# Optimization experiments

Measured on AMD Instinct MI355X. Metric: run time of the kernel, lower is better.

The kernel has to match this reference:

```python
import math
import jax, jax.numpy as jnp
import numpy as np

D_MODEL = 1024
N_HEADS = 16
HEAD_DIM = D_MODEL // N_HEADS
D_FF = 4096
N_LAYERS = 4
VOCAB = 2048
NUM_GROUPS = 15
CACHE_LEN = 17  # positions 0..16
EPS = 1e-6


def rmsnorm(x, w):
    return x * w * jax.lax.rsqrt(jnp.mean(x * x, axis=-1, keepdims=True) + EPS)


def rope(x, pos):
    # x: [S, H, hd], pos: [S] int
    hd = x.shape[-1]
    inv = 1.0 / (10000.0 ** (jnp.arange(0, hd, 2, dtype=jnp.float32) / hd))
    ang = pos[:, None].astype(jnp.float32) * inv  # [S, hd/2]
    cos = jnp.cos(ang)[:, None, :]
    sin = jnp.sin(ang)[:, None, :]
    x1, x2 = x[..., ::2], x[..., 1::2]
    return jnp.stack([x1 * cos - x2 * sin, x1 * sin + x2 * cos], axis=-1).reshape(x.shape)


def transformer_step(x, positions, kc, vc, wq, wk, wv, wo, w1, w2, w3, ln1, ln2, lnf):
    # x: [S, d]; positions: [S] contiguous; kc/vc: [L, H, T, hd] KV caches
    S = x.shape[0]
    cache_pos = jnp.arange(CACHE_LEN)
    mask = cache_pos[None, None, :] <= positions[None, :, None]  # causal vs cache [1,S,T]
    start = positions[0]
    for l in range(N_LAYERS):
        h = rmsnorm(x, ln1[l])
        q = rope((h @ wq[l].T).reshape(S, N_HEADS, HEAD_DIM), positions)
        k = rope((h @ wk[l].T).reshape(S, N_HEADS, HEAD_DIM), positions)
        v = (h @ wv[l].T).reshape(S, N_HEADS, HEAD_DIM)
        kc = jax.lax.dynamic_update_slice(kc, k.transpose(1, 0, 2)[None], (l, 0, start, 0))
        vc = jax.lax.dynamic_update_slice(vc, v.transpose(1, 0, 2)[None], (l, 0, start, 0))
        scores = jnp.einsum('shd,htd->hst', q, kc[l]) / math.sqrt(HEAD_DIM)
        p = jax.nn.softmax(jnp.where(mask, scores, -1e30), axis=-1)
        attn = jnp.einsum('hst,htd->shd', p, vc[l]).reshape(S, D_MODEL)
        x = x + attn @ wo[l].T
        h = rmsnorm(x, ln2[l])
        x = x + (jax.nn.silu(h @ w1[l].T) * (h @ w3[l].T)) @ w2[l].T
    return rmsnorm(x, lnf), kc, vc


def forward(talker_hidden, code_0_embed, wq, wk, wv, wo, w1, w2, w3, ln1, ln2, lnf, heads, embeds):
    kc = jnp.zeros((N_LAYERS, N_HEADS, CACHE_LEN, HEAD_DIM), jnp.float32)
    vc = kc
    # prefill: [talker_hidden; code_0_embed] at positions 0,1
    x0 = jnp.concatenate([talker_hidden[0], code_0_embed[0]], axis=0)  # [2, d]
    h, kc, vc = transformer_step(x0, jnp.arange(2), kc, vc, wq, wk, wv, wo, w1, w2, w3, ln1, ln2, lnf)
    hidden = h[-1:]  # last-token hidden [1, d]

    def step(carry, xs):
        hidden, kc, vc = carry
        head, etab, pos = xs  # head/etab: [V, d]
        logits = hidden @ head.T          # [1, V]
        code = jnp.argmax(logits, axis=-1)  # [1]
        emb = etab[code]                   # [1, d]
        nh, kc, vc = transformer_step(emb, pos[None], kc, vc, wq, wk, wv, wo, w1, w2, w3, ln1, ln2, lnf)
        return (nh, kc, vc), (logits[0], emb[0])

    (_, _, _), (all_logits, embs) = jax.lax.scan(
        step, (hidden, kc, vc), (heads, embeds, jnp.arange(2, 2 + NUM_GROUPS)))
    embed_sum = code_0_embed.reshape(-1) + embs.sum(0)
    return all_logits, embed_sum  # [15, V], [d]


def setup_inputs() -> dict:
    key = jax.random.key(0)
    ks = jax.random.split(key, 16)
    s = 0.02
    f32 = jnp.float32
    return {
        'talker_hidden': jax.random.normal(ks[0], (1, 1, D_MODEL), f32),
        'code_0_embed': jax.random.normal(ks[1], (1, 1, D_MODEL), f32),
        'wq': jax.random.normal(ks[2], (N_LAYERS, D_MODEL, D_MODEL), f32) * s,
        'wk': jax.random.normal(ks[3], (N_LAYERS, D_MODEL, D_MODEL), f32) * s,
        'wv': jax.random.normal(ks[4], (N_LAYERS, D_MODEL, D_MODEL), f32) * s,
        'wo': jax.random.normal(ks[5], (N_LAYERS, D_MODEL, D_MODEL), f32) * s,
        'w1': jax.random.normal(ks[6], (N_LAYERS, D_FF, D_MODEL), f32) * s,
        'w2': jax.random.normal(ks[7], (N_LAYERS, D_MODEL, D_FF), f32) * s,
        'w3': jax.random.normal(ks[8], (N_LAYERS, D_FF, D_MODEL), f32) * s,
        'ln1': jnp.ones((N_LAYERS, D_MODEL), f32),
        'ln2': jnp.ones((N_LAYERS, D_MODEL), f32),
        'lnf': jnp.ones((D_MODEL,), f32),
        'heads': jax.random.normal(ks[9], (NUM_GROUPS, VOCAB, D_MODEL), f32) * s,
        'embeds': jax.random.normal(ks[10], (NUM_GROUPS, VOCAB, D_MODEL), f32) * s,
    }


def reference(talker_hidden, code_0_embed, wq, wk, wv, wo, w1, w2, w3, ln1, ln2, lnf, heads, embeds):
    return forward(talker_hidden, code_0_embed, wq, wk, wv, wo, w1, w2, w3, ln1, ln2, lnf, heads, embeds)
```

## Files before the change

### kernel.cpp

```cpp
#include <hip/hip_runtime.h>
#include <math.h>

#define D_MODEL 1024
#define N_HEADS 16
#define HEAD_DIM 64
#define D_FF 4096
#define N_LAYERS 4
#define VOCAB 2048
#define NUM_GROUPS 15
#define CACHE_LEN 17
#define EPS 1e-6f
#define NB 256
#define NT 1024

typedef unsigned short ushort8v __attribute__((ext_vector_type(8)));

__device__ __forceinline__ float ldc(const float* p) {
  return __hip_atomic_load((float*)p, __ATOMIC_RELAXED, __HIP_MEMORY_SCOPE_AGENT);
}
__device__ __forceinline__ void stc(float* p, float v) {
  __hip_atomic_store(p, v, __ATOMIC_RELAXED, __HIP_MEMORY_SCOPE_AGENT);
}
__device__ __forceinline__ void stc2(float* p, float a, float b) {
  union { unsigned long long u; float2 f; } c;
  c.f = make_float2(a, b);
  __hip_atomic_store((unsigned long long*)p, c.u, __ATOMIC_RELAXED,
                     __HIP_MEMORY_SCOPE_AGENT);
}
__device__ __forceinline__ void stc_u64(unsigned long long* p, unsigned long long v) {
  __hip_atomic_store(p, v, __ATOMIC_RELAXED, __HIP_MEMORY_SCOPE_AGENT);
}
__device__ __forceinline__ unsigned ldu(const unsigned* p) {
  return __hip_atomic_load((unsigned*)p, __ATOMIC_RELAXED, __HIP_MEMORY_SCOPE_AGENT);
}

__device__ __forceinline__ float bf2f(unsigned short u) {
  union { unsigned int i; float f; } c;
  c.i = ((unsigned int)u) << 16;
  return c.f;
}
__device__ __forceinline__ unsigned short f2bf(float f) {
  union { float f; unsigned int i; } c;
  c.f = f;
  unsigned int r = (c.i + 0x7fffu + ((c.i >> 16) & 1u)) >> 16;
  return (unsigned short)r;
}

__device__ __forceinline__ float wred(float v) {
#pragma unroll
  for (int o = 32; o > 0; o >>= 1) v += __shfl_xor(v, o, 64);
  return v;
}
__device__ __forceinline__ float wredmax(float v) {
#pragma unroll
  for (int o = 32; o > 0; o >>= 1) v = fmaxf(v, __shfl_xor(v, o, 64));
  return v;
}

__device__ __forceinline__ void gsync_begin(unsigned* flags, unsigned gen) {
  __syncthreads();
  if (threadIdx.x == 0)
    __hip_atomic_store(flags + (size_t)blockIdx.x * 16u, gen, __ATOMIC_RELAXED,
                       __HIP_MEMORY_SCOPE_AGENT);
}
__device__ __forceinline__ void gsync_end(unsigned* flags, unsigned gen) {
  if (threadIdx.x < 64) {
    const unsigned* f = flags + (size_t)threadIdx.x * 16u;
    for (;;) {
      unsigned a0 = ldu(f);
      unsigned a1 = ldu(f + 64 * 16);
      unsigned a2 = ldu(f + 128 * 16);
      unsigned a3 = ldu(f + 192 * 16);
      if (a0 >= gen && a1 >= gen && a2 >= gen && a3 >= gen) break;
      __builtin_amdgcn_s_sleep(1);
    }
  }
  __syncthreads();
}

template <int BF>
__device__ __forceinline__ void ldsub(const unsigned short* Wb, const float* Wf,
                                      size_t row, int nsub, int it, ushort8v& ob,
                                      float* of) {
  int lane = threadIdx.x & 63;
  if constexpr (BF) {
    ob = ((const ushort8v*)Wb)[(row * nsub + it) * 64 + lane];
  } else {
    const float* p = Wf + row * (size_t)nsub * 512 + it * 512 + lane;
#pragma unroll
    for (int c = 0; c < 8; ++c) of[c] = p[c * 64];
  }
}

template <int BF>
__device__ __forceinline__ float dsub(const ushort8v& wb, const float* wf,
                                      const float* a8) {
  float acc = 0.f;
  if constexpr (BF) {
#pragma unroll
    for (int c = 0; c < 8; ++c) acc = fmaf(bf2f(wb[c]), a8[c], acc);
  } else {
#pragma unroll
    for (int c = 0; c < 8; ++c) acc = fmaf(wf[c], a8[c], acc);
  }
  return acc;
}

__device__ __forceinline__ void act8(const float* __restrict__ seg, float* a8) {
  int lane = threadIdx.x & 63;
#pragma unroll
  for (int c = 0; c < 8; ++c) a8[c] = seg[c * 64 + lane];
}

__device__ __forceinline__ void conv_t(const float* __restrict__ src,
                                       unsigned long long* __restrict__ dst,
                                       size_t rows, int wprl) {
  size_t nw = rows << wprl;
  size_t stride = (size_t)NB * NT;
  for (size_t w = (size_t)blockIdx.x * NT + threadIdx.x; w < nw; w += stride) {
    size_t row = w >> wprl;
    int rem = (int)(w & (((size_t)1 << wprl) - 1));
    int it = rem >> 6, ln_ = rem & 63;
    const float* p = src + (row << (wprl + 3)) + it * 512 + ln_;
    unsigned long long lo = 0, hi = 0;
#pragma unroll
    for (int c = 0; c < 4; ++c)
      lo |= (unsigned long long)f2bf(p[c * 64]) << (16 * c);
#pragma unroll
    for (int c = 0; c < 4; ++c)
      hi |= (unsigned long long)f2bf(p[(c + 4) * 64]) << (16 * c);
    stc_u64(dst + 2 * w, lo);
    stc_u64(dst + 2 * w + 1, hi);
  }
}

struct KParams {
  const float *th, *c0, *ln1, *ln2, *lnf, *heads, *embeds;
  const float *fwq, *fwk, *fwv, *fwo, *fw1, *fw2, *fw3;
  unsigned short *bwq, *bwk, *bwv, *bwo, *bw1, *bw2, *bw3;
  float *out, *x, *qb, *ff, *lbuf, *esum, *kc, *vc;
  unsigned* bar;
};

__global__ void k_zero(unsigned* bar) {
  int i = blockIdx.x * 1024 + threadIdx.x;
  if (i < 4096) bar[i] = 0;
}

template <int BF>
__global__ __launch_bounds__(NT, 1) void mega(KParams P) {
  __shared__ float s_attn[2 * D_MODEL];
  __shared__ float s_xn[2 * D_MODEL];
  __shared__ float s_ff[2 * D_FF];
  __shared__ float s_red[32];
  __shared__ float s_bval[16];
  __shared__ int s_bidx[16];
  __shared__ int s_code;
  float* s_qb = s_ff;

  unsigned gen = 0;
  const int tid = threadIdx.x, lane = tid & 63, wv_ = tid >> 6;
  const int bid = blockIdx.x;

  const int R_q = bid * 12 + wv_;
  const int m_q = R_q >> 10;
  const int rr_q = R_q & 1023;
  const int h_q = rr_q >> 6, dd_q = rr_q & 63;
  const int wo_r = wv_ >> 1, wo_h = wv_ & 1;
  const int ff_j = bid * 16 + wv_;
  const int w2_r = wv_ >> 2, w2_q = wv_ & 3;
  const int lg_r = wv_ >> 1, lg_h = wv_ & 1;

  ushort8v pQ0{}, pQ1{}, pWo{}, p10{}, p11{}, p30{}, p31{}, pW20{}, pW21{};
  float pQf[16], pWof[8], p1f[16], p3f[16], pW2f[16], pHf[8];

  const size_t QKVO = (size_t)N_LAYERS * D_MODEL * D_MODEL;
  const size_t FFW = (size_t)N_LAYERS * D_FF * D_MODEL;

  if constexpr (BF) {
    conv_t(P.fwq, (unsigned long long*)P.bwq, N_LAYERS * D_MODEL, 7);
    conv_t(P.fwk, (unsigned long long*)P.bwk, N_LAYERS * D_MODEL, 7);
    conv_t(P.fwv, (unsigned long long*)P.bwv, N_LAYERS * D_MODEL, 7);
    conv_t(P.fwo, (unsigned long long*)P.bwo, N_LAYERS * D_MODEL, 7);
    conv_t(P.fw1, (unsigned long long*)P.bw1, (size_t)N_LAYERS * D_FF, 7);
    conv_t(P.fw3, (unsigned long long*)P.bw3, (size_t)N_LAYERS * D_FF, 7);
    conv_t(P.fw2, (unsigned long long*)P.bw2, N_LAYERS * D_MODEL, 9);
  }
  if (bid == 0) {
    stc(&P.x[tid], P.th[tid]);
    stc(&P.x[D_MODEL + tid], P.c0[tid]);
    P.esum[tid] = P.c0[tid];
  }

  auto stage_xn = [&](int s, const float* src, bool coh, const float* ln) {
    float v = coh ? ldc(src + tid) : src[tid];
    float p = wred(v * v);
    if ((tid & 63) == 0) s_red[tid >> 6] = p;
    __syncthreads();
    float t = 0.f;
#pragma unroll
    for (int w = 0; w < 16; ++w) t += s_red[w];
    float sc = rsqrtf(t * (1.f / D_MODEL) + EPS);
    s_xn[s * D_MODEL + tid] = v * ln[tid] * sc;
    __syncthreads();
  };

  auto block_argmax = [&]() -> int {
    float v0 = ldc(P.lbuf + tid);
    int i0 = tid;
    float v1 = ldc(P.lbuf + tid + 1024);
    if (v1 > v0) { v0 = v1; i0 = tid + 1024; }
#pragma unroll
    for (int o = 32; o > 0; o >>= 1) {
      float v2 = __shfl_xor(v0, o, 64);
      int i2 = __shfl_xor(i0, o, 64);
      if (v2 > v0 || (v2 == v0 && i2 < i0)) { v0 = v2; i0 = i2; }
    }
    if (lane == 0) { s_bval[wv_] = v0; s_bidx[wv_] = i0; }
    __syncthreads();
    if (tid == 0) {
      float b = s_bval[0];
      int bi = s_bidx[0];
#pragma unroll
      for (int w = 1; w < 16; ++w) {
        float v = s_bval[w];
        int i = s_bidx[w];
        if (v > b || (v == b && i < bi)) { b = v; bi = i; }
      }
      s_code = bi;
    }
    __syncthreads();
    return s_code;
  };

  auto pf_qkv = [&](int l) {
    const unsigned short* Wb = (m_q == 0) ? P.bwq : (m_q == 1) ? P.bwk : P.bwv;
    const float* Wf = (m_q == 0) ? P.fwq : (m_q == 1) ? P.fwk : P.fwv;
    size_t row = (size_t)l * D_MODEL + rr_q;
    ldsub<BF>(Wb, Wf, row, 2, 0, pQ0, pQf);
    ldsub<BF>(Wb, Wf, row, 2, 1, pQ1, pQf + 8);
  };
  auto pf_head = [&](const float* head) {
    const float* hp = head + (size_t)(bid * 8 + lg_r) * D_MODEL + lg_h * 512 + lane;
#pragma unroll
    for (int c = 0; c < 8; ++c) pHf[c] = hp[c * 64];
  };

  auto qkv_phase = [&](int S, int start, float* kcl, float* vcl) {
    for (int s = 0; s < S; ++s) {
      if (wv_ < 12) {
        float a0[8], a1[8];
        act8(s_xn + s * D_MODEL, a0);
        act8(s_xn + s * D_MODEL + 512, a1);
        float d = wred(dsub<BF>(pQ0, pQf, a0) + dsub<BF>(pQ1, pQf + 8, a1));
        if (m_q >= 2) {
          if (lane == 0) stc(&vcl[(h_q * CACHE_LEN + start + s) * HEAD_DIM + dd_q], d);
        } else if (lane == 0) {
          s_red[s * 16 + wv_] = d;
        }
      }
    }
    __syncthreads();
    if (wv_ < 12 && m_q < 2 && !(rr_q & 1) && lane == 0) {
      int i = dd_q >> 1;
      float inv = powf(10000.f, -(float)(2 * i) / 64.f);
      for (int s = 0; s < S; ++s) {
        int pos = start + s;
        float d0 = s_red[s * 16 + wv_];
        float d1 = s_red[s * 16 + wv_ + 1];
        float ang = (float)pos * inv;
        float c = cosf(ang), sn = sinf(ang);
        float o0 = d0 * c - d1 * sn;
        float o1 = d0 * sn + d1 * c;
        if (m_q == 0) stc2(&P.qb[s * D_MODEL + rr_q], o0, o1);
        else stc2(&kcl[(h_q * CACHE_LEN + pos) * HEAD_DIM + dd_q], o0, o1);
      }
    }
  };

  auto aw_phase = [&](int S, int start, const float* kcl, const float* vcl) {
    for (int s = 0; s < S; ++s) s_qb[s * D_MODEL + tid] = ldc(&P.qb[s * D_MODEL + tid]);
    __syncthreads();
    int h = wv_;
    for (int s = 0; s < S; ++s) {
      int pos = start + s;
      float scv = -1e30f;
      if (lane <= pos) {
        const float4* krow =
            (const float4*)(kcl + (size_t)(h * CACHE_LEN + lane) * HEAD_DIM);
        const float* q4 = s_qb + s * D_MODEL + h * HEAD_DIM;
        float acc = 0.f;
#pragma unroll
        for (int d0 = 0; d0 < 16; ++d0) {
          float4 k = krow[d0];
          acc = fmaf(k.x, q4[d0 * 4], fmaf(k.y, q4[d0 * 4 + 1],
                fmaf(k.z, q4[d0 * 4 + 2], fmaf(k.w, q4[d0 * 4 + 3], acc))));
        }
        scv = acc * 0.125f;
      }
      float mx = wredmax(scv);
      float e = (lane <= pos) ? expf(scv - mx) : 0.f;
      float den = wred(e);
      float pr = e / den;
      float pv = 0.f;
#pragma unroll
      for (int t = 0; t < CACHE_LEN; ++t) {
        if (t <= pos)
          pv = fmaf(__shfl(pr, t, 64),
                    vcl[(size_t)(h * CACHE_LEN + t) * HEAD_DIM + lane], pv);
      }
      s_attn[s * D_MODEL + h * HEAD_DIM + lane] = pv;
    }
    __syncthreads();
    if (wv_ < 8) {
      for (int s = 0; s < S; ++s) {
        float a8[8];
        act8(s_attn + s * D_MODEL + wo_h * 512, a8);
        float part = wred(dsub<BF>(pWo, pWof, a8));
        if (lane == 0) s_red[s * 16 + wv_] = part;
      }
    }
    __syncthreads();
    if (tid < 4 * S) {
      int s = tid >> 2, rr = tid & 3;
      float* xp = &P.x[s * D_MODEL + bid * 4 + rr];
      stc(xp, ldc(xp) + s_red[s * 16 + rr * 2] + s_red[s * 16 + rr * 2 + 1]);
    }
  };

  auto ffup_phase = [&](int S) {
    for (int s = 0; s < S; ++s) {
      float a0[8], a1[8];
      act8(s_xn + s * D_MODEL, a0);
      act8(s_xn + s * D_MODEL + 512, a1);
      float g = wred(dsub<BF>(p10, p1f, a0) + dsub<BF>(p11, p1f + 8, a1));
      float u = wred(dsub<BF>(p30, p3f, a0) + dsub<BF>(p31, p3f + 8, a1));
      if (lane == 0) stc(&P.ff[s * D_FF + ff_j], (g / (1.f + expf(-g))) * u);
    }
  };

  auto ffdown_phase = [&](int S) {
    for (int s = 0; s < S; ++s) {
#pragma unroll
      for (int k = 0; k < 4; ++k)
        s_ff[s * D_FF + k * 1024 + tid] = ldc(&P.ff[s * D_FF + k * 1024 + tid]);
    }
    __syncthreads();
    for (int s = 0; s < S; ++s) {
      float a0[8], a1[8];
      act8(s_ff + s * D_FF + w2_q * 1024, a0);
      act8(s_ff + s * D_FF + w2_q * 1024 + 512, a1);
      float part = wred(dsub<BF>(pW20, pW2f, a0) + dsub<BF>(pW21, pW2f + 8, a1));
      if (lane == 0) s_red[s * 16 + wv_] = part;
    }
    __syncthreads();
    if (tid < 4 * S) {
      int s = tid >> 2, rr2 = tid & 3;
      float v = s_red[s * 16 + rr2 * 4] + s_red[s * 16 + rr2 * 4 + 1] +
                s_red[s * 16 + rr2 * 4 + 2] + s_red[s * 16 + rr2 * 4 + 3];
      float* xp = &P.x[s * D_MODEL + bid * 4 + rr2];
      stc(xp, ldc(xp) + v);
    }
  };

  auto logits_phase = [&](int row, float* outg) {
    stage_xn(0, P.x + row * D_MODEL, true, P.lnf);
    float a8[8];
    act8(s_xn + lg_h * 512, a8);
    float d = 0.f;
#pragma unroll
    for (int c = 0; c < 8; ++c) d = fmaf(pHf[c], a8[c], d);
    d = wred(d);
    if (lane == 0) s_red[wv_] = d;
    __syncthreads();
    if (tid < 8) {
      float v = s_red[tid * 2] + s_red[tid * 2 + 1];
      stc(&P.lbuf[bid * 8 + tid], v);
      outg[bid * 8 + tid] = v;
    }
  };

  auto full_step = [&](int S, int start, bool am, const float* etab,
                       const float* next_head) {
    for (int l = 0; l < N_LAYERS; ++l) {
      float* kcl = P.kc + (size_t)l * N_HEADS * CACHE_LEN * HEAD_DIM;
      float* vcl = P.vc + (size_t)l * N_HEADS * CACHE_LEN * HEAD_DIM;
      const float* ln1l = P.ln1 + l * D_MODEL;
      if (am && l == 0) {
        int code = block_argmax();
        const float* hin = etab + (size_t)code * D_MODEL;
        if (bid == 0) {
          float e = hin[tid];
          stc(&P.x[tid], e);
          P.esum[tid] += e;
        }
        stage_xn(0, hin, false, ln1l);
      } else {
        for (int s = 0; s < S; ++s) stage_xn(s, P.x + s * D_MODEL, true, ln1l);
      }
      qkv_phase(S, start, kcl, vcl);
      ++gen;
      gsync_begin(P.bar, gen);
      if (wv_ < 8)
        ldsub<BF>(P.bwo, P.fwo, (size_t)l * D_MODEL + bid * 4 + wo_r, 2, wo_h, pWo, pWof);
      __builtin_amdgcn_sched_barrier(0);
      gsync_end(P.bar, gen);
      aw_phase(S, start, kcl, vcl);
      ++gen;
      gsync_begin(P.bar, gen);
      {
        size_t r1 = (size_t)l * D_FF + ff_j;
        ldsub<BF>(P.bw1, P.fw1, r1, 2, 0, p10, p1f);
        ldsub<BF>(P.bw1, P.fw1, r1, 2, 1, p11, p1f + 8);
        ldsub<BF>(P.bw3, P.fw3, r1, 2, 0, p30, p3f);
        ldsub<BF>(P.bw3, P.fw3, r1, 2, 1, p31, p3f + 8);
      }
      __builtin_amdgcn_sched_barrier(0);
      gsync_end(P.bar, gen);
      {
        const float* ln2l = P.ln2 + l * D_MODEL;
        for (int s = 0; s < S; ++s) stage_xn(s, P.x + s * D_MODEL, true, ln2l);
      }
      ffup_phase(S);
      ++gen;
      gsync_begin(P.bar, gen);
      {
        size_t r2 = (size_t)l * D_MODEL + bid * 4 + w2_r;
        ldsub<BF>(P.bw2, P.fw2, r2, 8, w2_q * 2, pW20, pW2f);
        ldsub<BF>(P.bw2, P.fw2, r2, 8, w2_q * 2 + 1, pW21, pW2f + 8);
      }
      __builtin_amdgcn_sched_barrier(0);
      gsync_end(P.bar, gen);
      ffdown_phase(S);
      ++gen;
      gsync_begin(P.bar, gen);
      if (l < N_LAYERS - 1) {
        if (wv_ < 12) pf_qkv(l + 1);
      } else {
        pf_head(next_head);
      }
      __builtin_amdgcn_sched_barrier(0);
      gsync_end(P.bar, gen);
    }
  };

  ++gen;
  gsync_begin(P.bar, gen);
  gsync_end(P.bar, gen);
  if (wv_ < 12) pf_qkv(0);

  full_step(2, 0, false, nullptr, P.heads);

  for (int g = 0; g < NUM_GROUPS; ++g) {
    logits_phase(g == 0 ? 1 : 0, P.out + (size_t)g * VOCAB);
    ++gen;
    gsync_begin(P.bar, gen);
    if (wv_ < 12) pf_qkv(0);
    __builtin_amdgcn_sched_barrier(0);
    gsync_end(P.bar, gen);
    if (g < NUM_GROUPS - 1) {
      full_step(1, 2 + g, true, P.embeds + (size_t)g * VOCAB * D_MODEL,
                P.heads + (size_t)(g + 1) * VOCAB * D_MODEL);
    } else {
      if (bid == 0) {
        int code = block_argmax();
        const float* emb =
            P.embeds + (size_t)g * VOCAB * D_MODEL + (size_t)code * D_MODEL;
        P.out[(size_t)NUM_GROUPS * VOCAB + tid] = P.esum[tid] + emb[tid];
      }
    }
  }
}

extern "C" void kernel_launch(void* const* d_in, const int* in_sizes, int n_in,
                              void* d_out, int out_size, void* d_ws, size_t ws_size,
                              hipStream_t stream) {
  KParams P;
  P.th = (const float*)d_in[0];
  P.c0 = (const float*)d_in[1];
  P.fwq = (const float*)d_in[2];
  P.fwk = (const float*)d_in[3];
  P.fwv = (const float*)d_in[4];
  P.fwo = (const float*)d_in[5];
  P.fw1 = (const float*)d_in[6];
  P.fw2 = (const float*)d_in[7];
  P.fw3 = (const float*)d_in[8];
  P.ln1 = (const float*)d_in[9];
  P.ln2 = (const float*)d_in[10];
  P.lnf = (const float*)d_in[11];
  P.heads = (const float*)d_in[12];
  P.embeds = (const float*)d_in[13];
  P.out = (float*)d_out;

  const size_t QKVO = (size_t)N_LAYERS * D_MODEL * D_MODEL;
  const size_t FFW = (size_t)N_LAYERS * D_FF * D_MODEL;
  const size_t W_ELEMS = 4 * QKVO + 3 * FFW;
  const size_t SCRATCH = 2048 + 2048 + 8192 + 2048 + 1024 + 69632 + 69632;
  const size_t NEED = W_ELEMS * 2 + SCRATCH * 4 + 4096 * 4;

  float* fs;
  int use_bf16 = (ws_size >= NEED);
  if (use_bf16) {
    unsigned short* wb = (unsigned short*)d_ws;
    P.bwq = wb;
    P.bwk = wb + QKVO;
    P.bwv = wb + 2 * QKVO;
    P.bwo = wb + 3 * QKVO;
    P.bw1 = wb + 4 * QKVO;
    P.bw3 = wb + 4 * QKVO + FFW;
    P.bw2 = wb + 4 * QKVO + 2 * FFW;
    fs = (float*)(wb + W_ELEMS);
  } else {
    P.bwq = P.bwk = P.bwv = P.bwo = P.bw1 = P.bw2 = P.bw3 = nullptr;
    fs = (float*)d_ws;
  }
  P.x = fs;
  P.qb = fs + 2048;
  P.ff = fs + 4096;
  P.lbuf = fs + 12288;
  P.esum = fs + 14336;
  P.kc = fs + 15360;
  P.vc = fs + 84992;
  P.bar = (unsigned*)(fs + SCRATCH);

  k_zero<<<4, 1024, 0, stream>>>(P.bar);
  void* args[] = {&P};
  if (use_bf16) {
    hipLaunchCooperativeKernel(reinterpret_cast<void*>(&mega<1>), dim3(NB), dim3(NT),
                               args, 0, stream);
  } else {
    hipLaunchCooperativeKernel(reinterpret_cast<void*>(&mega<0>), dim3(NB), dim3(NT),
                               args, 0, stream);
  }
}
```

Measured before the change: 1.676 ms.

## Parallelize grid barrier polling and pre-reduce argmax per block

The grid barrier now has 256 threads each poll one block flag instead of 64 threads polling four flags each. The logits phase now reduces its 8 logits to a per-block max and index, so the later argmax reads only 256 candidates instead of 2048. The attention phase lets each wave load only its own head's slice of q into shared memory, which removes a __syncthreads. The risks are more polling traffic from the barrier and subtle changes in tie-breaking or visibility for the per-wave q load.

```diff
diff --git a/kernel.cpp b/kernel.cpp
--- a/kernel.cpp
+++ b/kernel.cpp
@@ -64,16 +64,9 @@
                        __HIP_MEMORY_SCOPE_AGENT);
 }
 __device__ __forceinline__ void gsync_end(unsigned* flags, unsigned gen) {
-  if (threadIdx.x < 64) {
+  if (threadIdx.x < NB) {
     const unsigned* f = flags + (size_t)threadIdx.x * 16u;
-    for (;;) {
-      unsigned a0 = ldu(f);
-      unsigned a1 = ldu(f + 64 * 16);
-      unsigned a2 = ldu(f + 128 * 16);
-      unsigned a3 = ldu(f + 192 * 16);
-      if (a0 >= gen && a1 >= gen && a2 >= gen && a3 >= gen) break;
-      __builtin_amdgcn_s_sleep(1);
-    }
+    while (ldu(f) < gen) __builtin_amdgcn_s_sleep(1);
   }
   __syncthreads();
 }
@@ -138,7 +131,7 @@
   const float *th, *c0, *ln1, *ln2, *lnf, *heads, *embeds;
   const float *fwq, *fwk, *fwv, *fwo, *fw1, *fw2, *fw3;
   unsigned short *bwq, *bwk, *bwv, *bwo, *bw1, *bw2, *bw3;
-  float *out, *x, *qb, *ff, *lbuf, *esum, *kc, *vc;
+  float *out, *x, *qb, *ff, *pbv, *pbi, *esum, *kc, *vc;
   unsigned* bar;
 };
 
@@ -206,10 +199,12 @@
   };
 
   auto block_argmax = [&]() -> int {
-    float v0 = ldc(P.lbuf + tid);
-    int i0 = tid;
-    float v1 = ldc(P.lbuf + tid + 1024);
-    if (v1 > v0) { v0 = v1; i0 = tid + 1024; }
+    float v0 = -1e38f;
+    int i0 = 0x7fffffff;
+    if (tid < NB) {
+      v0 = ldc(P.pbv + tid);
+      i0 = (int)ldc(P.pbi + tid);
+    }
 #pragma unroll
     for (int o = 32; o > 0; o >>= 1) {
       float v2 = __shfl_xor(v0, o, 64);
@@ -222,7 +217,7 @@
       float b = s_bval[0];
       int bi = s_bidx[0];
 #pragma unroll
-      for (int w = 1; w < 16; ++w) {
+      for (int w = 1; w < 4; ++w) {
         float v = s_bval[w];
         int i = s_bidx[w];
         if (v > b || (v == b && i < bi)) { b = v; bi = i; }
@@ -279,9 +274,10 @@
   };
 
   auto aw_phase = [&](int S, int start, const float* kcl, const float* vcl) {
-    for (int s = 0; s < S; ++s) s_qb[s * D_MODEL + tid] = ldc(&P.qb[s * D_MODEL + tid]);
-    __syncthreads();
     int h = wv_;
+    for (int s = 0; s < S; ++s)
+      s_qb[s * D_MODEL + h * HEAD_DIM + lane] =
+          ldc(&P.qb[s * D_MODEL + h * HEAD_DIM + lane]);
     for (int s = 0; s < S; ++s) {
       int pos = start + s;
       float scv = -1e30f;
@@ -375,8 +371,20 @@
     __syncthreads();
     if (tid < 8) {
       float v = s_red[tid * 2] + s_red[tid * 2 + 1];
-      stc(&P.lbuf[bid * 8 + tid], v);
       outg[bid * 8 + tid] = v;
+      s_red[16 + tid] = v;
+    }
+    __syncthreads();
+    if (tid == 0) {
+      float b = s_red[16];
+      int bi = 0;
+#pragma unroll
+      for (int j = 1; j < 8; ++j) {
+        float v = s_red[16 + j];
+        if (v > b) { b = v; bi = j; }
+      }
+      stc(&P.pbv[bid], b);
+      stc(&P.pbi[bid], (float)(bid * 8 + bi));
     }
   };
 
@@ -495,7 +503,7 @@
   const size_t QKVO = (size_t)N_LAYERS * D_MODEL * D_MODEL;
   const size_t FFW = (size_t)N_LAYERS * D_FF * D_MODEL;
   const size_t W_ELEMS = 4 * QKVO + 3 * FFW;
-  const size_t SCRATCH = 2048 + 2048 + 8192 + 2048 + 1024 + 69632 + 69632;
+  const size_t SCRATCH = 2048 + 2048 + 8192 + 256 + 256 + 1024 + 69632 + 69632;
   const size_t NEED = W_ELEMS * 2 + SCRATCH * 4 + 4096 * 4;
 
   float* fs;
@@ -517,10 +525,11 @@
   P.x = fs;
   P.qb = fs + 2048;
   P.ff = fs + 4096;
-  P.lbuf = fs + 12288;
-  P.esum = fs + 14336;
-  P.kc = fs + 15360;
-  P.vc = fs + 84992;
+  P.pbv = fs + 12288;
+  P.pbi = fs + 12544;
+  P.esum = fs + 12800;
+  P.kc = fs + 13824;
+  P.vc = fs + 83456;
   P.bar = (unsigned*)(fs + SCRATCH);
 
   k_zero<<<4, 1024, 0, stream>>>(P.bar);
```

Result: faster. 1.606 ms (median of 2 runs) (-4.2%).
